# Performance work log

Hardware: AMD Instinct MI355X
Metric: run time of the kernel (lower is better)

Reference implementation:

```python
import jax, jax.numpy as jnp
import numpy as np

N_NODES, N_EDGES, CH, FEAT = 20000, 320000, 256, 118


def setup_inputs() -> dict:
    key = jax.random.key(0)
    ks = jax.random.split(key, 8)
    x = jax.random.uniform(ks[0], (N_NODES, FEAT), dtype=jnp.float32)
    edge_index = jax.random.randint(ks[1], (2, N_EDGES), 0, N_NODES, dtype=jnp.int64)
    s = 0.05
    W_embed = jax.random.normal(ks[2], (FEAT, CH), dtype=jnp.float32) * s
    b_embed = jnp.zeros((CH,), jnp.float32)
    W1 = jax.random.normal(ks[3], (CH, CH), dtype=jnp.float32) * s
    b1 = jnp.zeros((CH,), jnp.float32)
    W2 = jax.random.normal(ks[4], (CH, CH), dtype=jnp.float32) * s
    b2 = jnp.zeros((CH,), jnp.float32)
    return {"x": x, "edge_index": edge_index, "W_embed": W_embed, "b_embed": b_embed,
            "W1": W1, "b1": b1, "W2": W2, "b2": b2}


def reference(x, edge_index, W_embed, b_embed, W1, b1, W2, b2):
    n = x.shape[0]
    # node embedding: Linear(118 -> C)
    h = x @ W_embed + b_embed  # [N, C]
    src, dst = edge_index[0], edge_index[1]
    # message: gather x_j per edge, dense1 + exact GELU (dropout = identity in eval)
    msg = jax.nn.gelu(h[src] @ W1 + b1, approximate=False)  # [E, C]
    # mean aggregation into destination nodes
    agg = jax.ops.segment_sum(msg, dst, num_segments=n)  # [N, C]
    cnt = jax.ops.segment_sum(jnp.ones((msg.shape[0],), msg.dtype), dst, num_segments=n)
    agg = agg / jnp.maximum(cnt, 1.0)[:, None]
    # update: dense2 + exact GELU
    out = jax.nn.gelu(agg @ W2 + b2, approximate=False)  # [N, C]
    # final mean over channel dim
    return out.mean(axis=1)  # [N]
```

## Files before the change

kernel.cpp:

```cpp
#include <hip/hip_runtime.h>
#include <math.h>

#define N_NODES 20000
#define N_EDGES 320000
#define CH      256
#define FEAT    118
#define CAP     48

typedef float    f32x4 __attribute__((ext_vector_type(4)));
typedef short    s16x8 __attribute__((ext_vector_type(8)));
typedef _Float16 f16x4 __attribute__((ext_vector_type(4)));
typedef _Float16 f16x8 __attribute__((ext_vector_type(8)));
typedef unsigned short u16;

union Frag { s16x8 v; u16 u[8]; };

__device__ __forceinline__ float gelu_exact(float x) {
    return 0.5f * x * (1.0f + erff(x * 0.70710678118654752f));
}
__device__ __forceinline__ u16 f2bf(float f) {
    unsigned u = __float_as_uint(f);
    u = (u + 0x7FFFu + ((u >> 16) & 1u)) >> 16;
    return (u16)u;
}
__device__ __forceinline__ float bf2f(u16 h) { return __uint_as_float(((unsigned)h) << 16); }

__device__ __forceinline__ void cvt_split(f16x8 a, s16x8& hi, s16x8& lo) {
    Frag H, L;
    #pragma unroll
    for (int e = 0; e < 8; e++) {
        float v = (float)a[e];
        u16 h = f2bf(v);
        H.u[e] = h; L.u[e] = f2bf(v - bf2f(h));
    }
    hi = H.v; lo = L.v;
}

__global__ __launch_bounds__(256) void prep(const float* __restrict__ x,
                                            const int* __restrict__ ei,
                                            const float* __restrict__ We,
                                            const float* __restrict__ be,
                                            const float* __restrict__ W1,
                                            const float* __restrict__ b1,
                                            const float* __restrict__ W2,
                                            u16* __restrict__ xh, u16* __restrict__ xl,
                                            int* __restrict__ cnt, int* __restrict__ bins,
                                            u16* __restrict__ w2h, u16* __restrict__ w2l,
                                            u16* __restrict__ wch, u16* __restrict__ wcl,
                                            float* __restrict__ bc) {
    const int b = blockIdx.x, tid = threadIdx.x;
    if (b < 1250) {
        int fid = b * 256 + tid;
        int lane = fid & 63, ks = (fid >> 6) & 3, mt = fid >> 8;
        int row = mt * 16 + (lane & 15);
        int k0 = ks * 32 + (lane >> 4) * 8;
        Frag hi, lo;
        #pragma unroll
        for (int j = 0; j < 8; j++) {
            int k = k0 + j;
            float v = (k < FEAT) ? x[(size_t)row * FEAT + k] : 0.0f;
            u16 h = f2bf(v);
            hi.u[j] = h; lo.u[j] = f2bf(v - bf2f(h));
        }
        ((s16x8*)xh)[fid] = hi.v;
        ((s16x8*)xl)[fid] = lo.v;
    } else if (b < 2500) {
        int e = (b - 1250) * 256 + tid;
        int s = ei[e];
        int d = ei[N_EDGES + e];
        int p = atomicAdd(&cnt[d], 1);
        if (p < CAP) bins[(size_t)d * CAP + p] = s;
    } else if (b < 2532) {
        int fid = (b - 2500) * 256 + tid;
        int lane = fid & 63, ks = (fid >> 6) & 7, nt = fid >> 9;
        int n = nt * 16 + (lane & 15);
        int k0 = ks * 32 + (lane >> 4) * 8;
        Frag hi, lo;
        #pragma unroll
        for (int j = 0; j < 8; j++) {
            float v = W2[(size_t)(k0 + j) * 256 + n];
            u16 h = f2bf(v);
            hi.u[j] = h; lo.u[j] = f2bf(v - bf2f(h));
        }
        ((s16x8*)w2h)[fid] = hi.v;
        ((s16x8*)w2l)[fid] = lo.v;
    } else {
        int f = b - 2532;
        int n = tid;
        if (f < 128) {
            float acc = 0.0f;
            if (f < FEAT) {
                const float* wr = We + (size_t)f * 256;
                #pragma unroll 8
                for (int c = 0; c < 256; c++) acc += wr[c] * W1[(size_t)c * 256 + n];
            }
            int nt = n >> 4, lm = n & 15, ks = f >> 5, q = (f >> 3) & 3, j = f & 7;
            size_t idx = (((size_t)nt * 4 + ks) * 64 + q * 16 + lm) * 8 + j;
            u16 h = f2bf(acc);
            wch[idx] = h;
            wcl[idx] = f2bf(acc - bf2f(h));
        } else {
            float acc = b1[n];
            #pragma unroll 8
            for (int c = 0; c < 256; c++) acc += be[c] * W1[(size_t)c * 256 + n];
            bc[n] = acc;
        }
    }
}

__global__ __launch_bounds__(256) void gemm_main(const u16* __restrict__ Ah_, const u16* __restrict__ Al_,
                                                 const u16* __restrict__ Bh_, const u16* __restrict__ Bl_,
                                                 const float* __restrict__ bias,
                                                 _Float16* __restrict__ Mout) {
    __shared__ _Float16 Ls[32][256];
    const int tid = threadIdx.x, wave = tid >> 6, lane = tid & 63;
    const int quad = lane >> 4, lm = lane & 15;
    const int mt0 = blockIdx.x * 2, nt0 = wave * 4;
    const s16x8* Ah = (const s16x8*)Ah_; const s16x8* Al = (const s16x8*)Al_;
    const s16x8* Bh = (const s16x8*)Bh_; const s16x8* Bl = (const s16x8*)Bl_;
    f32x4 acc[2][4];
    #pragma unroll
    for (int mi = 0; mi < 2; mi++)
        #pragma unroll
        for (int t = 0; t < 4; t++) acc[mi][t] = f32x4{0.f, 0.f, 0.f, 0.f};
    #pragma unroll
    for (int ks = 0; ks < 4; ks++) {
        s16x8 a0h = Ah[((size_t)(mt0 + 0) * 4 + ks) * 64 + lane];
        s16x8 a0l = Al[((size_t)(mt0 + 0) * 4 + ks) * 64 + lane];
        s16x8 a1h = Ah[((size_t)(mt0 + 1) * 4 + ks) * 64 + lane];
        s16x8 a1l = Al[((size_t)(mt0 + 1) * 4 + ks) * 64 + lane];
        #pragma unroll
        for (int t = 0; t < 4; t++) {
            s16x8 bh = Bh[((size_t)(nt0 + t) * 4 + ks) * 64 + lane];
            s16x8 bl = Bl[((size_t)(nt0 + t) * 4 + ks) * 64 + lane];
            acc[0][t] = __builtin_amdgcn_mfma_f32_16x16x32_bf16(a0h, bh, acc[0][t], 0, 0, 0);
            acc[0][t] = __builtin_amdgcn_mfma_f32_16x16x32_bf16(a0l, bh, acc[0][t], 0, 0, 0);
            acc[0][t] = __builtin_amdgcn_mfma_f32_16x16x32_bf16(a0h, bl, acc[0][t], 0, 0, 0);
            acc[1][t] = __builtin_amdgcn_mfma_f32_16x16x32_bf16(a1h, bh, acc[1][t], 0, 0, 0);
            acc[1][t] = __builtin_amdgcn_mfma_f32_16x16x32_bf16(a1l, bh, acc[1][t], 0, 0, 0);
            acc[1][t] = __builtin_amdgcn_mfma_f32_16x16x32_bf16(a1h, bl, acc[1][t], 0, 0, 0);
        }
    }
    #pragma unroll
    for (int t = 0; t < 4; t++) {
        float bn = bias[(nt0 + t) * 16 + lm];
        #pragma unroll
        for (int mi = 0; mi < 2; mi++)
            #pragma unroll
            for (int r = 0; r < 4; r++)
                Ls[mi * 16 + quad * 4 + r][(nt0 + t) * 16 + lm] =
                    (_Float16)gelu_exact(acc[mi][t][r] + bn);
    }
    __syncthreads();
    s16x8* dst = (s16x8*)Mout + (size_t)blockIdx.x * 1024;
    const s16x8* src = (const s16x8*)&Ls[0][0];
    #pragma unroll
    for (int it = 0; it < 4; it++)
        dst[it * 256 + tid] = src[it * 256 + tid];
}

__global__ __launch_bounds__(256) void aggregate(const _Float16* __restrict__ M,
                                                 const int* __restrict__ cnt,
                                                 const int* __restrict__ bins,
                                                 _Float16* __restrict__ agg) {
    int node = (blockIdx.x * 256 + threadIdx.x) >> 6;
    int lane = threadIdx.x & 63;
    int c = cnt[node];
    int cc = min(c, CAP);
    int myid = (lane < CAP) ? bins[(size_t)node * CAP + lane] : 0;
    float a0 = 0.f, a1 = 0.f, a2 = 0.f, a3 = 0.f;
    for (int j = 0; j < cc; j += 8) {
        f16x4 v[8];
        #pragma unroll
        for (int u = 0; u < 8; u++) {
            int s = __shfl(myid, min(j + u, cc - 1), 64);
            v[u] = *(const f16x4*)(M + (size_t)s * CH + lane * 4);
        }
        #pragma unroll
        for (int u = 0; u < 8; u++) {
            if (j + u < cc) {
                a0 += (float)v[u].x; a1 += (float)v[u].y;
                a2 += (float)v[u].z; a3 += (float)v[u].w;
            }
        }
    }
    float inv = 1.0f / (float)max(c, 1);
    f16x4 o;
    o.x = (_Float16)(a0 * inv); o.y = (_Float16)(a1 * inv);
    o.z = (_Float16)(a2 * inv); o.w = (_Float16)(a3 * inv);
    *(f16x4*)(agg + (size_t)node * CH + lane * 4) = o;
}

#define LPITCH 264
__global__ __launch_bounds__(256) void gemm_mean(const _Float16* __restrict__ agg,
                                                 const u16* __restrict__ Bh_, const u16* __restrict__ Bl_,
                                                 const float* __restrict__ bias,
                                                 float* __restrict__ out) {
    __shared__ _Float16 Ls[32][LPITCH];
    __shared__ float part[4][32];
    const int tid = threadIdx.x, wave = tid >> 6, lane = tid & 63;
    const int quad = lane >> 4, lm = lane & 15;
    const int nt0 = wave * 4;
    {
        const f16x8* src = (const f16x8*)(agg + (size_t)blockIdx.x * 32 * CH);
        #pragma unroll
        for (int it = 0; it < 4; it++) {
            int id = it * 256 + tid;
            int row = id >> 5, seg = id & 31;
            *(f16x8*)&Ls[row][seg * 8] = src[id];
        }
    }
    __syncthreads();
    const s16x8* Bh = (const s16x8*)Bh_; const s16x8* Bl = (const s16x8*)Bl_;
    f32x4 acc[2][4];
    #pragma unroll
    for (int mi = 0; mi < 2; mi++)
        #pragma unroll
        for (int t = 0; t < 4; t++) acc[mi][t] = f32x4{0.f, 0.f, 0.f, 0.f};
    #pragma unroll
    for (int ks = 0; ks < 8; ks++) {
        int c0 = ks * 32 + quad * 8;
        s16x8 a0h, a0l, a1h, a1l;
        cvt_split(*(const f16x8*)&Ls[lm][c0],      a0h, a0l);
        cvt_split(*(const f16x8*)&Ls[16 + lm][c0], a1h, a1l);
        #pragma unroll
        for (int t = 0; t < 4; t++) {
            s16x8 bh = Bh[((size_t)(nt0 + t) * 8 + ks) * 64 + lane];
            s16x8 bl = Bl[((size_t)(nt0 + t) * 8 + ks) * 64 + lane];
            acc[0][t] = __builtin_amdgcn_mfma_f32_16x16x32_bf16(a0h, bh, acc[0][t], 0, 0, 0);
            acc[0][t] = __builtin_amdgcn_mfma_f32_16x16x32_bf16(a0l, bh, acc[0][t], 0, 0, 0);
            acc[0][t] = __builtin_amdgcn_mfma_f32_16x16x32_bf16(a0h, bl, acc[0][t], 0, 0, 0);
            acc[1][t] = __builtin_amdgcn_mfma_f32_16x16x32_bf16(a1h, bh, acc[1][t], 0, 0, 0);
            acc[1][t] = __builtin_amdgcn_mfma_f32_16x16x32_bf16(a1l, bh, acc[1][t], 0, 0, 0);
            acc[1][t] = __builtin_amdgcn_mfma_f32_16x16x32_bf16(a1h, bl, acc[1][t], 0, 0, 0);
        }
    }
    float p[2][4] = {{0.f,0.f,0.f,0.f},{0.f,0.f,0.f,0.f}};
    #pragma unroll
    for (int t = 0; t < 4; t++) {
        float bn = bias[(nt0 + t) * 16 + lm];
        #pragma unroll
        for (int mi = 0; mi < 2; mi++)
            #pragma unroll
            for (int r = 0; r < 4; r++)
                p[mi][r] += gelu_exact(acc[mi][t][r] + bn);
    }
    #pragma unroll
    for (int off = 1; off < 16; off <<= 1)
        #pragma unroll
        for (int mi = 0; mi < 2; mi++)
            #pragma unroll
            for (int r = 0; r < 4; r++)
                p[mi][r] += __shfl_xor(p[mi][r], off, 64);
    if (lm == 0)
        #pragma unroll
        for (int mi = 0; mi < 2; mi++)
            #pragma unroll
            for (int r = 0; r < 4; r++)
                part[wave][mi * 16 + quad * 4 + r] = p[mi][r];
    __syncthreads();
    if (tid < 32) {
        float s = part[0][tid] + part[1][tid] + part[2][tid] + part[3][tid];
        out[blockIdx.x * 32 + tid] = s * (1.0f / 256.0f);
    }
}

extern "C" void kernel_launch(void* const* d_in, const int* in_sizes, int n_in,
                              void* d_out, int out_size, void* d_ws, size_t ws_size,
                              hipStream_t stream) {
    const float* x  = (const float*)d_in[0];
    const int*   ei = (const int*)d_in[1];
    const float* We = (const float*)d_in[2];
    const float* be = (const float*)d_in[3];
    const float* W1 = (const float*)d_in[4];
    const float* b1 = (const float*)d_in[5];
    const float* W2 = (const float*)d_in[6];
    const float* b2 = (const float*)d_in[7];
    float* out = (float*)d_out;

    char* ws = (char*)d_ws;
    size_t off = 0;
    u16* xh = (u16*)(ws + off);
    _Float16* agg = (_Float16*)(ws + off);
    off += 5120000;
    u16* xl = (u16*)(ws + off); off += 5120000;
    _Float16* M = (_Float16*)(ws + off); off += 10240000;
    u16* wch = (u16*)(ws + off); off += 65536;
    u16* wcl = (u16*)(ws + off); off += 65536;
    u16* w2h = (u16*)(ws + off); off += 131072;
    u16* w2l = (u16*)(ws + off); off += 131072;
    float* bc = (float*)(ws + off); off += 1024;
    int* cnt  = (int*)(ws + off); off += N_NODES * 4;
    int* bins = (int*)(ws + off); off += (size_t)N_NODES * CAP * 4;

    hipMemsetAsync(cnt, 0, N_NODES * sizeof(int), stream);
    prep<<<2661, 256, 0, stream>>>(x, ei, We, be, W1, b1, W2,
                                   xh, xl, cnt, bins, w2h, w2l, wch, wcl, bc);
    gemm_main<<<N_NODES / 32, 256, 0, stream>>>(xh, xl, wch, wcl, bc, M);
    aggregate<<<N_NODES / 4, 256, 0, stream>>>(M, cnt, bins, agg);
    gemm_mean<<<N_NODES / 32, 256, 0, stream>>>(agg, w2h, w2l, b2, out);
}
```

Before: 158.6 us.

## Use fp16 MFMA with scaled split W2 and fragment-layout agg output

The second GEMM now runs on fp16 MFMA. The fp16 aggregate is the A operand directly, and W2 is split into an fp16 hi part plus a lo part scaled by 4096. The aggregate kernel writes its output straight into MFMA fragment layout, which removes the LDS staging and the per-element bf16 hi/lo conversion in gemm_mean. It also cuts the MFMA count from three to two per tile. Separately, gemm_main now uses 16-row blocks, doubling the grid, and the aggregate gather unroll drops from 8 to 4. The risks are small precision differences from fp16 W2 splitting and a less coalesced scattered write in aggregate.

```diff
diff --git a/kernel.cpp b/kernel.cpp
--- a/kernel.cpp
+++ b/kernel.cpp
@@ -13,7 +13,8 @@
 typedef _Float16 f16x8 __attribute__((ext_vector_type(8)));
 typedef unsigned short u16;
 
-union Frag { s16x8 v; u16 u[8]; };
+union Frag  { s16x8 v; u16 u[8]; };
+union FragH { f16x8 v; _Float16 h[8]; };
 
 __device__ __forceinline__ float gelu_exact(float x) {
     return 0.5f * x * (1.0f + erff(x * 0.70710678118654752f));
@@ -24,17 +25,6 @@
     return (u16)u;
 }
 __device__ __forceinline__ float bf2f(u16 h) { return __uint_as_float(((unsigned)h) << 16); }
-
-__device__ __forceinline__ void cvt_split(f16x8 a, s16x8& hi, s16x8& lo) {
-    Frag H, L;
-    #pragma unroll
-    for (int e = 0; e < 8; e++) {
-        float v = (float)a[e];
-        u16 h = f2bf(v);
-        H.u[e] = h; L.u[e] = f2bf(v - bf2f(h));
-    }
-    hi = H.v; lo = L.v;
-}
 
 __global__ __launch_bounds__(256) void prep(const float* __restrict__ x,
                                             const int* __restrict__ ei,
@@ -45,7 +35,7 @@
                                             const float* __restrict__ W2,
                                             u16* __restrict__ xh, u16* __restrict__ xl,
                                             int* __restrict__ cnt, int* __restrict__ bins,
-                                            u16* __restrict__ w2h, u16* __restrict__ w2l,
+                                            _Float16* __restrict__ w2h, _Float16* __restrict__ w2l,
                                             u16* __restrict__ wch, u16* __restrict__ wcl,
                                             float* __restrict__ bc) {
     const int b = blockIdx.x, tid = threadIdx.x;
@@ -75,15 +65,16 @@
         int lane = fid & 63, ks = (fid >> 6) & 7, nt = fid >> 9;
         int n = nt * 16 + (lane & 15);
         int k0 = ks * 32 + (lane >> 4) * 8;
-        Frag hi, lo;
+        FragH hi, lo;
         #pragma unroll
         for (int j = 0; j < 8; j++) {
             float v = W2[(size_t)(k0 + j) * 256 + n];
-            u16 h = f2bf(v);
-            hi.u[j] = h; lo.u[j] = f2bf(v - bf2f(h));
-        }
-        ((s16x8*)w2h)[fid] = hi.v;
-        ((s16x8*)w2l)[fid] = lo.v;
+            _Float16 h = (_Float16)v;
+            hi.h[j] = h;
+            lo.h[j] = (_Float16)((v - (float)h) * 4096.0f);
+        }
+        ((f16x8*)w2h)[fid] = hi.v;
+        ((f16x8*)w2l)[fid] = lo.v;
     } else {
         int f = b - 2532;
         int n = tid;
@@ -112,72 +103,59 @@
                                                  const u16* __restrict__ Bh_, const u16* __restrict__ Bl_,
                                                  const float* __restrict__ bias,
                                                  _Float16* __restrict__ Mout) {
-    __shared__ _Float16 Ls[32][256];
+    __shared__ _Float16 Ls[16][256];
     const int tid = threadIdx.x, wave = tid >> 6, lane = tid & 63;
     const int quad = lane >> 4, lm = lane & 15;
-    const int mt0 = blockIdx.x * 2, nt0 = wave * 4;
+    const int mt = blockIdx.x, nt0 = wave * 4;
     const s16x8* Ah = (const s16x8*)Ah_; const s16x8* Al = (const s16x8*)Al_;
     const s16x8* Bh = (const s16x8*)Bh_; const s16x8* Bl = (const s16x8*)Bl_;
-    f32x4 acc[2][4];
-    #pragma unroll
-    for (int mi = 0; mi < 2; mi++)
-        #pragma unroll
-        for (int t = 0; t < 4; t++) acc[mi][t] = f32x4{0.f, 0.f, 0.f, 0.f};
+    f32x4 acc[4] = {f32x4{0,0,0,0}, f32x4{0,0,0,0}, f32x4{0,0,0,0}, f32x4{0,0,0,0}};
     #pragma unroll
     for (int ks = 0; ks < 4; ks++) {
-        s16x8 a0h = Ah[((size_t)(mt0 + 0) * 4 + ks) * 64 + lane];
-        s16x8 a0l = Al[((size_t)(mt0 + 0) * 4 + ks) * 64 + lane];
-        s16x8 a1h = Ah[((size_t)(mt0 + 1) * 4 + ks) * 64 + lane];
-        s16x8 a1l = Al[((size_t)(mt0 + 1) * 4 + ks) * 64 + lane];
+        s16x8 a_h = Ah[((size_t)mt * 4 + ks) * 64 + lane];
+        s16x8 a_l = Al[((size_t)mt * 4 + ks) * 64 + lane];
         #pragma unroll
         for (int t = 0; t < 4; t++) {
             s16x8 bh = Bh[((size_t)(nt0 + t) * 4 + ks) * 64 + lane];
             s16x8 bl = Bl[((size_t)(nt0 + t) * 4 + ks) * 64 + lane];
-            acc[0][t] = __builtin_amdgcn_mfma_f32_16x16x32_bf16(a0h, bh, acc[0][t], 0, 0, 0);
-            acc[0][t] = __builtin_amdgcn_mfma_f32_16x16x32_bf16(a0l, bh, acc[0][t], 0, 0, 0);
-            acc[0][t] = __builtin_amdgcn_mfma_f32_16x16x32_bf16(a0h, bl, acc[0][t], 0, 0, 0);
-            acc[1][t] = __builtin_amdgcn_mfma_f32_16x16x32_bf16(a1h, bh, acc[1][t], 0, 0, 0);
-            acc[1][t] = __builtin_amdgcn_mfma_f32_16x16x32_bf16(a1l, bh, acc[1][t], 0, 0, 0);
-            acc[1][t] = __builtin_amdgcn_mfma_f32_16x16x32_bf16(a1h, bl, acc[1][t], 0, 0, 0);
+            acc[t] = __builtin_amdgcn_mfma_f32_16x16x32_bf16(a_h, bh, acc[t], 0, 0, 0);
+            acc[t] = __builtin_amdgcn_mfma_f32_16x16x32_bf16(a_l, bh, acc[t], 0, 0, 0);
+            acc[t] = __builtin_amdgcn_mfma_f32_16x16x32_bf16(a_h, bl, acc[t], 0, 0, 0);
         }
     }
     #pragma unroll
     for (int t = 0; t < 4; t++) {
         float bn = bias[(nt0 + t) * 16 + lm];
         #pragma unroll
-        for (int mi = 0; mi < 2; mi++)
-            #pragma unroll
-            for (int r = 0; r < 4; r++)
-                Ls[mi * 16 + quad * 4 + r][(nt0 + t) * 16 + lm] =
-                    (_Float16)gelu_exact(acc[mi][t][r] + bn);
+        for (int r = 0; r < 4; r++)
+            Ls[quad * 4 + r][(nt0 + t) * 16 + lm] = (_Float16)gelu_exact(acc[t][r] + bn);
     }
     __syncthreads();
-    s16x8* dst = (s16x8*)Mout + (size_t)blockIdx.x * 1024;
+    s16x8* dst = (s16x8*)Mout + (size_t)mt * 512;
     const s16x8* src = (const s16x8*)&Ls[0][0];
-    #pragma unroll
-    for (int it = 0; it < 4; it++)
-        dst[it * 256 + tid] = src[it * 256 + tid];
+    dst[tid]       = src[tid];
+    dst[256 + tid] = src[256 + tid];
 }
 
 __global__ __launch_bounds__(256) void aggregate(const _Float16* __restrict__ M,
                                                  const int* __restrict__ cnt,
                                                  const int* __restrict__ bins,
-                                                 _Float16* __restrict__ agg) {
+                                                 _Float16* __restrict__ aggf) {
     int node = (blockIdx.x * 256 + threadIdx.x) >> 6;
     int lane = threadIdx.x & 63;
     int c = cnt[node];
     int cc = min(c, CAP);
     int myid = (lane < CAP) ? bins[(size_t)node * CAP + lane] : 0;
     float a0 = 0.f, a1 = 0.f, a2 = 0.f, a3 = 0.f;
-    for (int j = 0; j < cc; j += 8) {
-        f16x4 v[8];
-        #pragma unroll
-        for (int u = 0; u < 8; u++) {
+    for (int j = 0; j < cc; j += 4) {
+        f16x4 v[4];
+        #pragma unroll
+        for (int u = 0; u < 4; u++) {
             int s = __shfl(myid, min(j + u, cc - 1), 64);
             v[u] = *(const f16x4*)(M + (size_t)s * CH + lane * 4);
         }
         #pragma unroll
-        for (int u = 0; u < 8; u++) {
+        for (int u = 0; u < 4; u++) {
             if (j + u < cc) {
                 a0 += (float)v[u].x; a1 += (float)v[u].y;
                 a2 += (float)v[u].z; a3 += (float)v[u].w;
@@ -188,51 +166,42 @@
     f16x4 o;
     o.x = (_Float16)(a0 * inv); o.y = (_Float16)(a1 * inv);
     o.z = (_Float16)(a2 * inv); o.w = (_Float16)(a3 * inv);
-    *(f16x4*)(agg + (size_t)node * CH + lane * 4) = o;
-}
-
-#define LPITCH 264
-__global__ __launch_bounds__(256) void gemm_mean(const _Float16* __restrict__ agg,
-                                                 const u16* __restrict__ Bh_, const u16* __restrict__ Bl_,
+    int mt = node >> 4, lm = node & 15;
+    int ks = lane >> 3, quad = (lane & 7) >> 1, j0 = (lane & 1) * 4;
+    size_t base = (((size_t)mt * 8 + ks) * 64 + quad * 16 + lm) * 8 + j0;
+    *(f16x4*)(aggf + base) = o;
+}
+
+__global__ __launch_bounds__(256) void gemm_mean(const _Float16* __restrict__ Af_,
+                                                 const _Float16* __restrict__ Bh_, const _Float16* __restrict__ Bl_,
                                                  const float* __restrict__ bias,
                                                  float* __restrict__ out) {
-    __shared__ _Float16 Ls[32][LPITCH];
     __shared__ float part[4][32];
     const int tid = threadIdx.x, wave = tid >> 6, lane = tid & 63;
     const int quad = lane >> 4, lm = lane & 15;
-    const int nt0 = wave * 4;
-    {
-        const f16x8* src = (const f16x8*)(agg + (size_t)blockIdx.x * 32 * CH);
-        #pragma unroll
-        for (int it = 0; it < 4; it++) {
-            int id = it * 256 + tid;
-            int row = id >> 5, seg = id & 31;
-            *(f16x8*)&Ls[row][seg * 8] = src[id];
-        }
-    }
-    __syncthreads();
-    const s16x8* Bh = (const s16x8*)Bh_; const s16x8* Bl = (const s16x8*)Bl_;
-    f32x4 acc[2][4];
+    const int mt0 = blockIdx.x * 2, nt0 = wave * 4;
+    const f16x8* Af = (const f16x8*)Af_;
+    const f16x8* Bh = (const f16x8*)Bh_; const f16x8* Bl = (const f16x8*)Bl_;
+    f32x4 acch[2][4], accl[2][4];
     #pragma unroll
     for (int mi = 0; mi < 2; mi++)
         #pragma unroll
-        for (int t = 0; t < 4; t++) acc[mi][t] = f32x4{0.f, 0.f, 0.f, 0.f};
+        for (int t = 0; t < 4; t++) {
+            acch[mi][t] = f32x4{0.f, 0.f, 0.f, 0.f};
+            accl[mi][t] = f32x4{0.f, 0.f, 0.f, 0.f};
+        }
     #pragma unroll
     for (int ks = 0; ks < 8; ks++) {
-        int c0 = ks * 32 + quad * 8;
-        s16x8 a0h, a0l, a1h, a1l;
-        cvt_split(*(const f16x8*)&Ls[lm][c0],      a0h, a0l);
-        cvt_split(*(const f16x8*)&Ls[16 + lm][c0], a1h, a1l);
+        f16x8 a0 = Af[((size_t)(mt0 + 0) * 8 + ks) * 64 + lane];
+        f16x8 a1 = Af[((size_t)(mt0 + 1) * 8 + ks) * 64 + lane];
         #pragma unroll
         for (int t = 0; t < 4; t++) {
-            s16x8 bh = Bh[((size_t)(nt0 + t) * 8 + ks) * 64 + lane];
-            s16x8 bl = Bl[((size_t)(nt0 + t) * 8 + ks) * 64 + lane];
-            acc[0][t] = __builtin_amdgcn_mfma_f32_16x16x32_bf16(a0h, bh, acc[0][t], 0, 0, 0);
-            acc[0][t] = __builtin_amdgcn_mfma_f32_16x16x32_bf16(a0l, bh, acc[0][t], 0, 0, 0);
-            acc[0][t] = __builtin_amdgcn_mfma_f32_16x16x32_bf16(a0h, bl, acc[0][t], 0, 0, 0);
-            acc[1][t] = __builtin_amdgcn_mfma_f32_16x16x32_bf16(a1h, bh, acc[1][t], 0, 0, 0);
-            acc[1][t] = __builtin_amdgcn_mfma_f32_16x16x32_bf16(a1l, bh, acc[1][t], 0, 0, 0);
-            acc[1][t] = __builtin_amdgcn_mfma_f32_16x16x32_bf16(a1h, bl, acc[1][t], 0, 0, 0);
+            f16x8 bh = Bh[((size_t)(nt0 + t) * 8 + ks) * 64 + lane];
+            f16x8 bl = Bl[((size_t)(nt0 + t) * 8 + ks) * 64 + lane];
+            acch[0][t] = __builtin_amdgcn_mfma_f32_16x16x32_f16(a0, bh, acch[0][t], 0, 0, 0);
+            accl[0][t] = __builtin_amdgcn_mfma_f32_16x16x32_f16(a0, bl, accl[0][t], 0, 0, 0);
+            acch[1][t] = __builtin_amdgcn_mfma_f32_16x16x32_f16(a1, bh, acch[1][t], 0, 0, 0);
+            accl[1][t] = __builtin_amdgcn_mfma_f32_16x16x32_f16(a1, bl, accl[1][t], 0, 0, 0);
         }
     }
     float p[2][4] = {{0.f,0.f,0.f,0.f},{0.f,0.f,0.f,0.f}};
@@ -243,7 +212,7 @@
         for (int mi = 0; mi < 2; mi++)
             #pragma unroll
             for (int r = 0; r < 4; r++)
-                p[mi][r] += gelu_exact(acc[mi][t][r] + bn);
+                p[mi][r] += gelu_exact(acch[mi][t][r] + accl[mi][t][r] * (1.0f / 4096.0f) + bn);
     }
     #pragma unroll
     for (int off = 1; off < 16; off <<= 1)
@@ -281,14 +250,14 @@
     char* ws = (char*)d_ws;
     size_t off = 0;
     u16* xh = (u16*)(ws + off);
-    _Float16* agg = (_Float16*)(ws + off);
+    _Float16* aggf = (_Float16*)(ws + off);
     off += 5120000;
     u16* xl = (u16*)(ws + off); off += 5120000;
     _Float16* M = (_Float16*)(ws + off); off += 10240000;
     u16* wch = (u16*)(ws + off); off += 65536;
     u16* wcl = (u16*)(ws + off); off += 65536;
-    u16* w2h = (u16*)(ws + off); off += 131072;
-    u16* w2l = (u16*)(ws + off); off += 131072;
+    _Float16* w2h = (_Float16*)(ws + off); off += 131072;
+    _Float16* w2l = (_Float16*)(ws + off); off += 131072;
     float* bc = (float*)(ws + off); off += 1024;
     int* cnt  = (int*)(ws + off); off += N_NODES * 4;
     int* bins = (int*)(ws + off); off += (size_t)N_NODES * CAP * 4;
@@ -296,7 +265,7 @@
     hipMemsetAsync(cnt, 0, N_NODES * sizeof(int), stream);
     prep<<<2661, 256, 0, stream>>>(x, ei, We, be, W1, b1, W2,
                                    xh, xl, cnt, bins, w2h, w2l, wch, wcl, bc);
-    gemm_main<<<N_NODES / 32, 256, 0, stream>>>(xh, xl, wch, wcl, bc, M);
-    aggregate<<<N_NODES / 4, 256, 0, stream>>>(M, cnt, bins, agg);
-    gemm_mean<<<N_NODES / 32, 256, 0, stream>>>(agg, w2h, w2l, b2, out);
-}
+    gemm_main<<<N_NODES / 16, 256, 0, stream>>>(xh, xl, wch, wcl, bc, M);
+    aggregate<<<N_NODES / 4, 256, 0, stream>>>(M, cnt, bins, aggf);
+    gemm_mean<<<N_NODES / 32, 256, 0, stream>>>(aggf, w2h, w2l, b2, out);
+}
```

Measured after the change: 154.7 us. 1.03x faster.
